# Kernel tuning notes

Hardware: AMD Instinct MI355X
Metric: run time of the kernel (lower is better)

The kernel has to match this reference:

```python
import jax, jax.numpy as jnp
import numpy as np


def setup_inputs() -> dict:
    key = jax.random.key(0)
    k1, k2, k3, k4 = jax.random.split(key, 4)
    B, S, TAGSET = 256, 256, 126
    T = TAGSET + 2  # includes START (T-2) and STOP (T-1)
    feats = jax.random.normal(k1, (B, S, T), dtype=jnp.float32)
    # gold tags only take real-tag values
    tags = jax.random.randint(k2, (B, S), 0, TAGSET).astype(jnp.int64)
    # prefix (length) mask, as required by length_mask = mask.sum(1)
    lengths = jax.random.randint(k3, (B,), S // 2, S + 1)
    mask = (jnp.arange(S)[None, :] < lengths[:, None]).astype(jnp.int32)
    # transitions param: matches init constraints of the module
    transitions = 0.1 * jax.random.normal(k4, (T, T), dtype=jnp.float32)
    transitions = transitions.at[:, T - 2].set(-1000.0)  # nothing -> START
    transitions = transitions.at[T - 1, :].set(-1000.0)  # STOP -> nothing
    return {"feats": feats, "transitions": transitions, "tags": tags, "mask": mask}


def _crf_nll(feats, transitions, tags, mask):
    B, S, T = feats.shape
    START, STOP = T - 2, T - 1
    feats_t = jnp.transpose(feats, (1, 0, 2))          # [S, B, T]
    mask_t = mask.T.astype(bool)                        # [S, B]

    # ---- log-partition (forward algorithm) ----
    # scores[t, b, i, j] = feats[t, b, j] + transitions[i, j]
    partition0 = feats_t[0] + transitions[START][None, :]  # [B, T]

    def step(partition, xs):
        feat, m = xs                                    # feat: [B, T], m: [B]
        # vals[b, i, j] = partition[b, i] + transitions[i, j] + feat[b, j]
        vals = partition[:, :, None] + transitions[None, :, :] + feat[:, None, :]
        new_p = jax.nn.logsumexp(vals, axis=1)          # [B, T]
        partition = jnp.where(m[:, None], new_p, partition)
        return partition, None

    partition, _ = jax.lax.scan(step, partition0, (feats_t[1:], mask_t[1:]))
    # final transition to STOP
    final_vals = partition[:, :, None] + transitions[None, :, :]  # [B, T, T]
    forward_score = jax.nn.logsumexp(final_vals, axis=1)[:, STOP].sum()

    # ---- gold path score ----
    prev = jnp.concatenate(
        [jnp.full((B, 1), START, dtype=tags.dtype), tags[:, :-1]], axis=1
    )                                                   # [B, S]
    emit = jnp.take_along_axis(feats, tags[:, :, None], axis=2)[:, :, 0]  # [B, S]
    trans = transitions[prev, tags]                     # [B, S]
    tg_energy = ((emit + trans) * mask.astype(feats.dtype)).sum()
    lengths = mask.sum(axis=1)                          # [B]
    end_ids = jnp.take_along_axis(tags, (lengths - 1)[:, None], axis=1)[:, 0]
    end_energy = transitions[end_ids, STOP].sum()
    gold_score = tg_energy + end_energy

    return forward_score - gold_score


def reference(feats, transitions, tags, mask):
    return _crf_nll(feats, transitions, tags, mask)
```

## Files before the change

kernel.cpp:

```cpp
#include <hip/hip_runtime.h>
#include <hip/hip_bf16.h>

#define B_ 256
#define S_ 256
#define T_ 128
#define START_ 126
#define STOP_ 127

typedef __attribute__((ext_vector_type(8))) short short8;
typedef __attribute__((ext_vector_type(4))) float f32x4;
typedef __attribute__((ext_vector_type(4))) int i32x4;

__device__ __forceinline__ unsigned short f2bf(float f) {
    unsigned u = __float_as_uint(f);
    unsigned r = (u + 0x7FFFu + ((u >> 16) & 1u)) >> 16;
    return (unsigned short)r;
}

__global__ __launch_bounds__(64, 1) void crf_fwd(
    const float* __restrict__ feats,
    const float* __restrict__ trans,
    const int*   __restrict__ tags,
    const int*   __restrict__ mask,
    float* __restrict__ out)
{
    const int b = blockIdx.x;
    const int l = threadIdx.x;
    const int g = l >> 4;
    const int c = l & 15;

    const float* fb = feats + (size_t)b * (S_ * T_);

    short8 bfrag[4][8];
    #pragma unroll
    for (int kt = 0; kt < 4; ++kt) {
        #pragma unroll
        for (int nt = 0; nt < 8; ++nt) {
            short8 f;
            #pragma unroll
            for (int e = 0; e < 8; ++e) {
                const int k = kt * 16 + 4 * g + (e >> 1) + 64 * (e & 1);
                f[e] = (short)f2bf(__expf(trans[k * T_ + nt * 16 + c]));
            }
            bfrag[kt][nt] = f;
        }
    }

    int cnt = 0;
    #pragma unroll
    for (int s4 = 0; s4 < 4; ++s4) cnt += mask[b * S_ + s4 * 64 + l];
    #pragma unroll
    for (int o = 32; o; o >>= 1) cnt += __shfl_xor(cnt, o, 64);
    const int len = cnt;

    float cf[16], nf[16];
    #pragma unroll
    for (int r = 0; r < 8; ++r) {
        cf[2 * r]     = fb[r * T_ + l];
        cf[2 * r + 1] = fb[r * T_ + 64 + l];
    }

    float u0 = __expf(cf[0] + trans[START_ * T_ + l]);
    float u1 = __expf(cf[1] + trans[START_ * T_ + 64 + l]);
    float M = 0.f;

    for (int blk = 0; blk < 32; ++blk) {
        if (blk + 1 < 32) {
            #pragma unroll
            for (int r = 0; r < 8; ++r) {
                nf[2 * r]     = fb[((blk + 1) * 8 + r) * T_ + l];
                nf[2 * r + 1] = fb[((blk + 1) * 8 + r) * T_ + 64 + l];
            }
        }
        #pragma unroll
        for (int r = 0; r < 8; ++r) {
            const int tt = blk * 8 + r;
            if (r == 0 && blk == 0) continue;
            if (tt >= len) goto done;
            {
                unsigned pk;
                asm("v_cvt_pk_bf16_f32 %0, %1, %2" : "=v"(pk) : "v"(u0), "v"(u1));
                i32x4 w[4];
                #pragma unroll
                for (int kt = 0; kt < 4; ++kt) {
                    #pragma unroll
                    for (int q = 0; q < 4; ++q) {
                        w[kt][q] = __builtin_amdgcn_ds_bpermute(
                            64 * kt + 16 * g + 4 * q, (int)pk);
                    }
                }
                f32x4 acc[8];
                #pragma unroll
                for (int n = 0; n < 8; ++n) acc[n] = (f32x4){0.f, 0.f, 0.f, 0.f};
                #pragma unroll
                for (int kt = 0; kt < 4; ++kt) {
                    const short8 a = *(const short8*)&w[kt];
                    #pragma unroll
                    for (int n = 0; n < 8; ++n)
                        acc[n] = __builtin_amdgcn_mfma_f32_16x16x32_bf16(
                            a, bfrag[kt][n], acc[n], 0, 0, 0);
                }
                float lo0 = (g & 1) ? acc[1][0] : acc[0][0];
                float hi0 = (g & 1) ? acc[3][0] : acc[2][0];
                float v0  = (g & 2) ? hi0 : lo0;
                float lo1 = (g & 1) ? acc[5][0] : acc[4][0];
                float hi1 = (g & 1) ? acc[7][0] : acc[6][0];
                float v1  = (g & 2) ? hi1 : lo1;
                u0 = v0 * __expf(cf[2 * r]);
                u1 = v1 * __expf(cf[2 * r + 1]);
                if ((tt & 3) == 0) {
                    const float sc = __shfl(u0, 0, 64);
                    const float rs = 1.0f / sc;
                    u0 *= rs;
                    u1 *= rs;
                    M += __logf(sc);
                }
            }
        }
        if (blk + 1 < 32) {
            #pragma unroll
            for (int i = 0; i < 16; ++i) cf[i] = nf[i];
        }
    }
done: ;

    float v = u0 * __expf(trans[l * T_ + STOP_])
            + u1 * __expf(trans[(64 + l) * T_ + STOP_]);
    #pragma unroll
    for (int o = 32; o; o >>= 1) v += __shfl_xor(v, o, 64);
    const float fwd = M + __logf(v);

    float gg = 0.f;
    #pragma unroll
    for (int s4 = 0; s4 < 4; ++s4) {
        const int s = s4 * 64 + l;
        if (mask[b * S_ + s]) {
            const int tg = tags[b * S_ + s];
            const int pv = (s == 0) ? START_ : tags[b * S_ + s - 1];
            gg += fb[s * T_ + tg] + trans[pv * T_ + tg];
            if (s == len - 1) gg += trans[tg * T_ + STOP_];
        }
    }
    #pragma unroll
    for (int o = 32; o; o >>= 1) gg += __shfl_xor(gg, o, 64);

    if (l == 0) atomicAdd(out, fwd - gg);
}

extern "C" void kernel_launch(void* const* d_in, const int* in_sizes, int n_in,
                              void* d_out, int out_size, void* d_ws, size_t ws_size,
                              hipStream_t stream) {
    const float* feats = (const float*)d_in[0];
    const float* trans = (const float*)d_in[1];
    const int*   tags  = (const int*)d_in[2];
    const int*   mask  = (const int*)d_in[3];
    float* out = (float*)d_out;

    hipMemsetAsync(out, 0, sizeof(float), stream);
    crf_fwd<<<dim3(B_), dim3(64), 0, stream>>>(feats, trans, tags, mask, out);
}
```

Before: 191.6 us.

## Transpose MFMA operands so the partition vector stays in accumulator layout

Transposes the matrix product so the exp-transitions matrix becomes the A operand and the partition vector becomes the B operand. The MFMA outputs can then be repacked straight into the next step's B fragment, with no ds_bpermute shuffles or lane-select logic per step. Emissions are exponentiated ahead of time into a double-buffered LDS tile, eight timesteps at a time, with prefetch, so the serial loop only reads them. The trade-off is more accumulator values kept live and repacked per step, plus reliance on manual waitcnt ordering around LDS writes with no barrier.

```diff
diff --git a/kernel.cpp b/kernel.cpp
--- a/kernel.cpp
+++ b/kernel.cpp
@@ -13,8 +13,7 @@
 
 __device__ __forceinline__ unsigned short f2bf(float f) {
     unsigned u = __float_as_uint(f);
-    unsigned r = (u + 0x7FFFu + ((u >> 16) & 1u)) >> 16;
-    return (unsigned short)r;
+    return (unsigned short)((u + 0x7FFFu + ((u >> 16) & 1u)) >> 16);
 }
 
 __global__ __launch_bounds__(64, 1) void crf_fwd(
@@ -28,21 +27,22 @@
     const int l = threadIdx.x;
     const int g = l >> 4;
     const int c = l & 15;
-
     const float* fb = feats + (size_t)b * (S_ * T_);
 
-    short8 bfrag[4][8];
+    __shared__ float efb[2][8][T_];
+
+    short8 afrag[4][8];
     #pragma unroll
     for (int kt = 0; kt < 4; ++kt) {
         #pragma unroll
-        for (int nt = 0; nt < 8; ++nt) {
+        for (int rt = 0; rt < 8; ++rt) {
             short8 f;
             #pragma unroll
             for (int e = 0; e < 8; ++e) {
-                const int k = kt * 16 + 4 * g + (e >> 1) + 64 * (e & 1);
-                f[e] = (short)f2bf(__expf(trans[k * T_ + nt * 16 + c]));
-            }
-            bfrag[kt][nt] = f;
+                const int k = (2 * kt + (e & 1)) * 16 + 4 * g + (e >> 1);
+                f[e] = (short)f2bf(__expf(trans[k * T_ + rt * 16 + c]));
+            }
+            afrag[kt][rt] = f;
         }
     }
 
@@ -53,81 +53,136 @@
     for (int o = 32; o; o >>= 1) cnt += __shfl_xor(cnt, o, 64);
     const int len = cnt;
 
-    float cf[16], nf[16];
-    #pragma unroll
-    for (int r = 0; r < 8; ++r) {
-        cf[2 * r]     = fb[r * T_ + l];
-        cf[2 * r + 1] = fb[r * T_ + 64 + l];
-    }
-
-    float u0 = __expf(cf[0] + trans[START_ * T_ + l]);
-    float u1 = __expf(cf[1] + trans[START_ * T_ + 64 + l]);
+    {
+        const int row = l >> 3, cb = (l & 7) * 16;
+        #pragma unroll
+        for (int i = 0; i < 4; ++i) {
+            float4 v = *(const float4*)&fb[row * T_ + cb + 4 * i];
+            float4 e;
+            e.x = __expf(v.x); e.y = __expf(v.y);
+            e.z = __expf(v.z); e.w = __expf(v.w);
+            *(float4*)&efb[0][row][cb + 4 * i] = e;
+        }
+    }
+    asm volatile("s_waitcnt lgkmcnt(0)" ::: "memory");
+
+    float held[8][4];
+    #pragma unroll
+    for (int rt = 0; rt < 8; ++rt) {
+        #pragma unroll
+        for (int q = 0; q < 4; ++q) {
+            const int j = rt * 16 + 4 * g + q;
+            held[rt][q] = __expf(fb[j] + trans[START_ * T_ + j]);
+        }
+    }
     float M = 0.f;
 
-    for (int blk = 0; blk < 32; ++blk) {
-        if (blk + 1 < 32) {
-            #pragma unroll
-            for (int r = 0; r < 8; ++r) {
-                nf[2 * r]     = fb[((blk + 1) * 8 + r) * T_ + l];
-                nf[2 * r + 1] = fb[((blk + 1) * 8 + r) * T_ + 64 + l];
-            }
-        }
-        #pragma unroll
-        for (int r = 0; r < 8; ++r) {
-            const int tt = blk * 8 + r;
-            if (r == 0 && blk == 0) continue;
-            if (tt >= len) goto done;
-            {
-                unsigned pk;
-                asm("v_cvt_pk_bf16_f32 %0, %1, %2" : "=v"(pk) : "v"(u0), "v"(u1));
-                i32x4 w[4];
+    short8 bfrag[4];
+    #pragma unroll
+    for (int kt = 0; kt < 4; ++kt) {
+        i32x4 t4;
+        #pragma unroll
+        for (int q = 0; q < 4; ++q) {
+            unsigned r;
+            asm("v_cvt_pk_bf16_f32 %0, %1, %2" : "=v"(r)
+                : "v"(held[2 * kt][q]), "v"(held[2 * kt + 1][q]));
+            t4[q] = (int)r;
+        }
+        bfrag[kt] = *(short8*)&t4;
+    }
+
+    float4 pre4[4];
+    int pend = 0;
+    for (int t = 1; t < S_; ++t) {
+        if (t >= len) break;
+        const int bc = (t >> 3) & 1, tr = t & 7;
+
+        if (tr == 1) {
+            const int nb = (t >> 3) + 1;
+            if (nb < S_ / 8) {
+                const int row = l >> 3, cb = (l & 7) * 16;
                 #pragma unroll
-                for (int kt = 0; kt < 4; ++kt) {
-                    #pragma unroll
-                    for (int q = 0; q < 4; ++q) {
-                        w[kt][q] = __builtin_amdgcn_ds_bpermute(
-                            64 * kt + 16 * g + 4 * q, (int)pk);
-                    }
-                }
-                f32x4 acc[8];
+                for (int i = 0; i < 4; ++i)
+                    pre4[i] = *(const float4*)&fb[(nb * 8 + row) * T_ + cb + 4 * i];
+                pend = 1;
+            }
+        }
+
+        float4 ef4[8];
+        #pragma unroll
+        for (int rt = 0; rt < 8; ++rt)
+            ef4[rt] = *(const float4*)&efb[bc][tr][rt * 16 + 4 * g];
+
+        f32x4 acc[8];
+        #pragma unroll
+        for (int rt = 0; rt < 8; ++rt) acc[rt] = (f32x4){0.f, 0.f, 0.f, 0.f};
+        #pragma unroll
+        for (int kt = 0; kt < 4; ++kt) {
+            #pragma unroll
+            for (int rt = 0; rt < 8; ++rt)
+                acc[rt] = __builtin_amdgcn_mfma_f32_16x16x32_bf16(
+                    afrag[kt][rt], bfrag[kt], acc[rt], 0, 0, 0);
+        }
+
+        if (tr == 6 && pend) {
+            const int dst = ((t >> 3) + 1) & 1;
+            const int row = l >> 3, cb = (l & 7) * 16;
+            #pragma unroll
+            for (int i = 0; i < 4; ++i) {
+                float4 e;
+                e.x = __expf(pre4[i].x); e.y = __expf(pre4[i].y);
+                e.z = __expf(pre4[i].z); e.w = __expf(pre4[i].w);
+                *(float4*)&efb[dst][row][cb + 4 * i] = e;
+            }
+            pend = 0;
+            asm volatile("s_waitcnt lgkmcnt(0)" ::: "memory");
+        }
+
+        #pragma unroll
+        for (int rt = 0; rt < 8; ++rt) {
+            held[rt][0] = acc[rt][0] * ef4[rt].x;
+            held[rt][1] = acc[rt][1] * ef4[rt].y;
+            held[rt][2] = acc[rt][2] * ef4[rt].z;
+            held[rt][3] = acc[rt][3] * ef4[rt].w;
+        }
+
+        if ((t & 3) == 0) {
+            const float sc = __uint_as_float(
+                __builtin_amdgcn_readfirstlane(__float_as_uint(held[0][0])));
+            const float rs = 1.0f / sc;
+            #pragma unroll
+            for (int rt = 0; rt < 8; ++rt) {
                 #pragma unroll
-                for (int n = 0; n < 8; ++n) acc[n] = (f32x4){0.f, 0.f, 0.f, 0.f};
-                #pragma unroll
-                for (int kt = 0; kt < 4; ++kt) {
-                    const short8 a = *(const short8*)&w[kt];
-                    #pragma unroll
-                    for (int n = 0; n < 8; ++n)
-                        acc[n] = __builtin_amdgcn_mfma_f32_16x16x32_bf16(
-                            a, bfrag[kt][n], acc[n], 0, 0, 0);
-                }
-                float lo0 = (g & 1) ? acc[1][0] : acc[0][0];
-                float hi0 = (g & 1) ? acc[3][0] : acc[2][0];
-                float v0  = (g & 2) ? hi0 : lo0;
-                float lo1 = (g & 1) ? acc[5][0] : acc[4][0];
-                float hi1 = (g & 1) ? acc[7][0] : acc[6][0];
-                float v1  = (g & 2) ? hi1 : lo1;
-                u0 = v0 * __expf(cf[2 * r]);
-                u1 = v1 * __expf(cf[2 * r + 1]);
-                if ((tt & 3) == 0) {
-                    const float sc = __shfl(u0, 0, 64);
-                    const float rs = 1.0f / sc;
-                    u0 *= rs;
-                    u1 *= rs;
-                    M += __logf(sc);
-                }
-            }
-        }
-        if (blk + 1 < 32) {
-            #pragma unroll
-            for (int i = 0; i < 16; ++i) cf[i] = nf[i];
-        }
-    }
-done: ;
-
-    float v = u0 * __expf(trans[l * T_ + STOP_])
-            + u1 * __expf(trans[(64 + l) * T_ + STOP_]);
-    #pragma unroll
-    for (int o = 32; o; o >>= 1) v += __shfl_xor(v, o, 64);
+                for (int q = 0; q < 4; ++q) held[rt][q] *= rs;
+            }
+            M += __logf(sc);
+        }
+
+        #pragma unroll
+        for (int kt = 0; kt < 4; ++kt) {
+            i32x4 t4;
+            #pragma unroll
+            for (int q = 0; q < 4; ++q) {
+                unsigned r;
+                asm("v_cvt_pk_bf16_f32 %0, %1, %2" : "=v"(r)
+                    : "v"(held[2 * kt][q]), "v"(held[2 * kt + 1][q]));
+                t4[q] = (int)r;
+            }
+            bfrag[kt] = *(short8*)&t4;
+        }
+    }
+
+    float v = 0.f;
+    #pragma unroll
+    for (int rt = 0; rt < 8; ++rt) {
+        #pragma unroll
+        for (int q = 0; q < 4; ++q) {
+            const int j = rt * 16 + 4 * g + q;
+            v += held[rt][q] * __expf(trans[j * T_ + STOP_]);
+        }
+    }
+    v += __shfl_xor(v, 16, 64);
+    v += __shfl_xor(v, 32, 64);
     const float fwd = M + __logf(v);
 
     float gg = 0.f;
```

Result: slower. 201.3 us (+5.1%).

## Batch 16 sequences per block so MFMA N-dimension covers sequences

Applied to the files above, without the earlier changes.

Restructures the forward recursion so each 256-thread block processes 16 sequences at once. The transposed exp(transitions) is held as the MFMA A operand, and the 16 sequences' probability vectors form the B operand, staged in double-buffered LDS. Before, one sequence per wave wasted most of each MFMA on a broadcast vector. This cuts per-step MFMA count and replaces the bpermutes with LDS reads. In exchange it adds a block barrier every timestep, launches only 16 blocks, and runs the loop to the maximum length within the group.

```diff
diff --git a/kernel.cpp b/kernel.cpp
--- a/kernel.cpp
+++ b/kernel.cpp
@@ -6,145 +6,201 @@
 #define T_ 128
 #define START_ 126
 #define STOP_ 127
+#define NSEQ 16
+#define NBLK (B_ / NSEQ)
+#define LDS_K 136
 
 typedef __attribute__((ext_vector_type(8))) short short8;
 typedef __attribute__((ext_vector_type(4))) float f32x4;
-typedef __attribute__((ext_vector_type(4))) int i32x4;
 
 __device__ __forceinline__ unsigned short f2bf(float f) {
     unsigned u = __float_as_uint(f);
-    unsigned r = (u + 0x7FFFu + ((u >> 16) & 1u)) >> 16;
-    return (unsigned short)r;
-}
-
-__global__ __launch_bounds__(64, 1) void crf_fwd(
+    return (unsigned short)((u + 0x7FFFu + ((u >> 16) & 1u)) >> 16);
+}
+__device__ __forceinline__ unsigned cvt_pk(float lo, float hi) {
+    unsigned r;
+    asm("v_cvt_pk_bf16_f32 %0, %1, %2" : "=v"(r) : "v"(lo), "v"(hi));
+    return r;
+}
+
+__global__ __launch_bounds__(256, 1) void crf_fwd(
     const float* __restrict__ feats,
     const float* __restrict__ trans,
     const int*   __restrict__ tags,
     const int*   __restrict__ mask,
     float* __restrict__ out)
 {
-    const int b = blockIdx.x;
-    const int l = threadIdx.x;
-    const int g = l >> 4;
-    const int c = l & 15;
-
-    const float* fb = feats + (size_t)b * (S_ * T_);
-
-    short8 bfrag[4][8];
-    #pragma unroll
-    for (int kt = 0; kt < 4; ++kt) {
-        #pragma unroll
-        for (int nt = 0; nt < 8; ++nt) {
+    const int tid = threadIdx.x;
+    const int W = tid >> 6, l = tid & 63, g = l >> 4, c = l & 15;
+    const int blk = blockIdx.x;
+    const int seq = blk * NSEQ + c;
+    const float* fb = feats + (size_t)seq * (S_ * T_);
+
+    __shared__ __align__(16) unsigned short st[2][NSEQ][LDS_K];
+    __shared__ float scl[NSEQ];
+    __shared__ float wred[4][NSEQ];
+    __shared__ int   lens[NSEQ];
+
+    short8 af[2][4];
+    #pragma unroll
+    for (int rt = 0; rt < 2; ++rt) {
+        #pragma unroll
+        for (int kt = 0; kt < 4; ++kt) {
             short8 f;
             #pragma unroll
-            for (int e = 0; e < 8; ++e) {
-                const int k = kt * 16 + 4 * g + (e >> 1) + 64 * (e & 1);
-                f[e] = (short)f2bf(__expf(trans[k * T_ + nt * 16 + c]));
-            }
-            bfrag[kt][nt] = f;
-        }
-    }
-
-    int cnt = 0;
-    #pragma unroll
-    for (int s4 = 0; s4 < 4; ++s4) cnt += mask[b * S_ + s4 * 64 + l];
-    #pragma unroll
-    for (int o = 32; o; o >>= 1) cnt += __shfl_xor(cnt, o, 64);
-    const int len = cnt;
-
-    float cf[16], nf[16];
-    #pragma unroll
-    for (int r = 0; r < 8; ++r) {
-        cf[2 * r]     = fb[r * T_ + l];
-        cf[2 * r + 1] = fb[r * T_ + 64 + l];
-    }
-
-    float u0 = __expf(cf[0] + trans[START_ * T_ + l]);
-    float u1 = __expf(cf[1] + trans[START_ * T_ + 64 + l]);
-    float M = 0.f;
-
-    for (int blk = 0; blk < 32; ++blk) {
-        if (blk + 1 < 32) {
-            #pragma unroll
-            for (int r = 0; r < 8; ++r) {
-                nf[2 * r]     = fb[((blk + 1) * 8 + r) * T_ + l];
-                nf[2 * r + 1] = fb[((blk + 1) * 8 + r) * T_ + 64 + l];
-            }
-        }
-        #pragma unroll
-        for (int r = 0; r < 8; ++r) {
-            const int tt = blk * 8 + r;
-            if (r == 0 && blk == 0) continue;
-            if (tt >= len) goto done;
-            {
-                unsigned pk;
-                asm("v_cvt_pk_bf16_f32 %0, %1, %2" : "=v"(pk) : "v"(u0), "v"(u1));
-                i32x4 w[4];
+            for (int e = 0; e < 8; ++e)
+                f[e] = (short)f2bf(__expf(
+                    trans[(32 * kt + 8 * g + e) * T_ + 32 * W + 16 * rt + c]));
+            af[rt][kt] = f;
+        }
+    }
+
+    {
+        const int* mrow = mask + seq * S_ + (4 * W + g) * 16;
+        int p = 0;
+        #pragma unroll
+        for (int i = 0; i < 4; ++i) {
+            int4 m4 = *(const int4*)&mrow[4 * i];
+            p += m4.x + m4.y + m4.z + m4.w;
+        }
+        p += __shfl_xor(p, 16, 64);
+        p += __shfl_xor(p, 32, 64);
+        if (g == 0) wred[W][c] = (float)p;
+    }
+    __syncthreads();
+    const int len_c = (int)(wred[0][c] + wred[1][c] + wred[2][c] + wred[3][c]);
+    if (W == 0 && g == 0) lens[c] = len_c;
+    int lm = len_c;
+    #pragma unroll
+    for (int o = 1; o < 16; o <<= 1) lm = max(lm, __shfl_xor(lm, o, 64));
+
+    float held[2][4], ets[2][4], M = 0.f;
+    #pragma unroll
+    for (int rt = 0; rt < 2; ++rt) {
+        #pragma unroll
+        for (int q = 0; q < 4; ++q) {
+            const int j = 32 * W + 16 * rt + 4 * g + q;
+            held[rt][q] = __expf(fb[j] + trans[START_ * T_ + j]);
+            ets[rt][q]  = __expf(trans[j * T_ + STOP_]);
+        }
+    }
+    #pragma unroll
+    for (int rt = 0; rt < 2; ++rt) {
+        const unsigned r0 = cvt_pk(held[rt][0], held[rt][1]);
+        const unsigned r1 = cvt_pk(held[rt][2], held[rt][3]);
+        *(uint2*)&st[0][c][32 * W + 16 * rt + 4 * g] = make_uint2(r0, r1);
+    }
+
+    float efO[2][4], efE[2][4];
+    #pragma unroll
+    for (int rt = 0; rt < 2; ++rt) {
+        #pragma unroll
+        for (int q = 0; q < 4; ++q) {
+            const int j = 32 * W + 16 * rt + 4 * g + q;
+            efO[rt][q] = fb[1 * T_ + j];
+            efE[rt][q] = fb[2 * T_ + j];
+        }
+    }
+    __syncthreads();
+
+    for (int t = 1; t < lm; ++t) {
+        const int p = (t - 1) & 1;
+        const short8 bf0 = *(const short8*)&st[p][c][ 0 + 8 * g];
+        const short8 bf1 = *(const short8*)&st[p][c][32 + 8 * g];
+        const short8 bf2 = *(const short8*)&st[p][c][64 + 8 * g];
+        const short8 bf3 = *(const short8*)&st[p][c][96 + 8 * g];
+        float sc = 1.0f;
+        if ((t & 3) == 0) sc = scl[c];
+
+        float fe[2][4];
+        const int tn = (t + 2 < S_) ? t + 2 : S_ - 1;
+        if (t & 1) {
+            #pragma unroll
+            for (int rt = 0; rt < 2; ++rt)
                 #pragma unroll
-                for (int kt = 0; kt < 4; ++kt) {
-                    #pragma unroll
-                    for (int q = 0; q < 4; ++q) {
-                        w[kt][q] = __builtin_amdgcn_ds_bpermute(
-                            64 * kt + 16 * g + 4 * q, (int)pk);
-                    }
+                for (int q = 0; q < 4; ++q) {
+                    fe[rt][q] = __expf(efO[rt][q]);
+                    efO[rt][q] = fb[tn * T_ + 32 * W + 16 * rt + 4 * g + q];
                 }
-                f32x4 acc[8];
+        } else {
+            #pragma unroll
+            for (int rt = 0; rt < 2; ++rt)
                 #pragma unroll
-                for (int n = 0; n < 8; ++n) acc[n] = (f32x4){0.f, 0.f, 0.f, 0.f};
+                for (int q = 0; q < 4; ++q) {
+                    fe[rt][q] = __expf(efE[rt][q]);
+                    efE[rt][q] = fb[tn * T_ + 32 * W + 16 * rt + 4 * g + q];
+                }
+        }
+
+        f32x4 a0 = {0.f, 0.f, 0.f, 0.f}, a1 = {0.f, 0.f, 0.f, 0.f};
+        a0 = __builtin_amdgcn_mfma_f32_16x16x32_bf16(af[0][0], bf0, a0, 0, 0, 0);
+        a1 = __builtin_amdgcn_mfma_f32_16x16x32_bf16(af[1][0], bf0, a1, 0, 0, 0);
+        a0 = __builtin_amdgcn_mfma_f32_16x16x32_bf16(af[0][1], bf1, a0, 0, 0, 0);
+        a1 = __builtin_amdgcn_mfma_f32_16x16x32_bf16(af[1][1], bf1, a1, 0, 0, 0);
+        a0 = __builtin_amdgcn_mfma_f32_16x16x32_bf16(af[0][2], bf2, a0, 0, 0, 0);
+        a1 = __builtin_amdgcn_mfma_f32_16x16x32_bf16(af[1][2], bf2, a1, 0, 0, 0);
+        a0 = __builtin_amdgcn_mfma_f32_16x16x32_bf16(af[0][3], bf3, a0, 0, 0, 0);
+        a1 = __builtin_amdgcn_mfma_f32_16x16x32_bf16(af[1][3], bf3, a1, 0, 0, 0);
+
+        const bool act = (t < len_c);
+        #pragma unroll
+        for (int q = 0; q < 4; ++q) {
+            held[0][q] = act ? a0[q] * fe[0][q] : held[0][q];
+            held[1][q] = act ? a1[q] * fe[1][q] : held[1][q];
+        }
+
+        if ((t & 3) == 0) {
+            const float rs = __builtin_amdgcn_rcpf(sc);
+            #pragma unroll
+            for (int rt = 0; rt < 2; ++rt)
                 #pragma unroll
-                for (int kt = 0; kt < 4; ++kt) {
-                    const short8 a = *(const short8*)&w[kt];
-                    #pragma unroll
-                    for (int n = 0; n < 8; ++n)
-                        acc[n] = __builtin_amdgcn_mfma_f32_16x16x32_bf16(
-                            a, bfrag[kt][n], acc[n], 0, 0, 0);
-                }
-                float lo0 = (g & 1) ? acc[1][0] : acc[0][0];
-                float hi0 = (g & 1) ? acc[3][0] : acc[2][0];
-                float v0  = (g & 2) ? hi0 : lo0;
-                float lo1 = (g & 1) ? acc[5][0] : acc[4][0];
-                float hi1 = (g & 1) ? acc[7][0] : acc[6][0];
-                float v1  = (g & 2) ? hi1 : lo1;
-                u0 = v0 * __expf(cf[2 * r]);
-                u1 = v1 * __expf(cf[2 * r + 1]);
-                if ((tt & 3) == 0) {
-                    const float sc = __shfl(u0, 0, 64);
-                    const float rs = 1.0f / sc;
-                    u0 *= rs;
-                    u1 *= rs;
-                    M += __logf(sc);
-                }
-            }
-        }
-        if (blk + 1 < 32) {
-            #pragma unroll
-            for (int i = 0; i < 16; ++i) cf[i] = nf[i];
-        }
-    }
-done: ;
-
-    float v = u0 * __expf(trans[l * T_ + STOP_])
-            + u1 * __expf(trans[(64 + l) * T_ + STOP_]);
-    #pragma unroll
-    for (int o = 32; o; o >>= 1) v += __shfl_xor(v, o, 64);
-    const float fwd = M + __logf(v);
-
-    float gg = 0.f;
-    #pragma unroll
-    for (int s4 = 0; s4 < 4; ++s4) {
-        const int s = s4 * 64 + l;
-        if (mask[b * S_ + s]) {
-            const int tg = tags[b * S_ + s];
-            const int pv = (s == 0) ? START_ : tags[b * S_ + s - 1];
-            gg += fb[s * T_ + tg] + trans[pv * T_ + tg];
-            if (s == len - 1) gg += trans[tg * T_ + STOP_];
-        }
-    }
-    #pragma unroll
-    for (int o = 32; o; o >>= 1) gg += __shfl_xor(gg, o, 64);
-
-    if (l == 0) atomicAdd(out, fwd - gg);
+                for (int q = 0; q < 4; ++q) held[rt][q] *= rs;
+            M += __logf(sc);
+        }
+        if ((t & 3) == 3 && W == 0 && g == 0) scl[c] = held[0][0];
+
+        #pragma unroll
+        for (int rt = 0; rt < 2; ++rt) {
+            const unsigned r0 = cvt_pk(held[rt][0], held[rt][1]);
+            const unsigned r1 = cvt_pk(held[rt][2], held[rt][3]);
+            *(uint2*)&st[t & 1][c][32 * W + 16 * rt + 4 * g] = make_uint2(r0, r1);
+        }
+        asm volatile("s_waitcnt lgkmcnt(0)\n\ts_barrier" ::: "memory");
+    }
+
+    float pv = 0.f;
+    #pragma unroll
+    for (int rt = 0; rt < 2; ++rt)
+        #pragma unroll
+        for (int q = 0; q < 4; ++q) pv += held[rt][q] * ets[rt][q];
+    pv += __shfl_xor(pv, 16, 64);
+    pv += __shfl_xor(pv, 32, 64);
+    if (g == 0) wred[W][c] = pv;
+    __syncthreads();
+    const float fwd_c =
+        M + __logf(wred[0][c] + wred[1][c] + wred[2][c] + wred[3][c]);
+
+    float part = (W == 0 && g == 0) ? fwd_c : 0.f;
+    const int s = tid;
+    #pragma unroll 4
+    for (int q2 = 0; q2 < NSEQ; ++q2) {
+        const int sq = blk * NSEQ + q2;
+        if (mask[sq * S_ + s]) {
+            const int tg  = tags[sq * S_ + s];
+            const int pvt = s ? tags[sq * S_ + s - 1] : START_;
+            float e = feats[(size_t)sq * (S_ * T_) + s * T_ + tg]
+                    + trans[pvt * T_ + tg];
+            if (s == lens[q2] - 1) e += trans[tg * T_ + STOP_];
+            part -= e;
+        }
+    }
+    #pragma unroll
+    for (int o = 32; o; o >>= 1) part += __shfl_down(part, o, 64);
+    __syncthreads();
+    if (l == 0) wred[0][W] = part;
+    __syncthreads();
+    if (tid == 0)
+        atomicAdd(out, wred[0][0] + wred[0][1] + wred[0][2] + wred[0][3]);
 }
 
 extern "C" void kernel_launch(void* const* d_in, const int* in_sizes, int n_in,
@@ -157,5 +213,5 @@
     float* out = (float*)d_out;
 
     hipMemsetAsync(out, 0, sizeof(float), stream);
-    crf_fwd<<<dim3(B_), dim3(64), 0, stream>>>(feats, trans, tags, mask, out);
-}
+    crf_fwd<<<dim3(NBLK), dim3(256), 0, stream>>>(feats, trans, tags, mask, out);
+}
```

Result: slower. 245.6 us (+28.2%).
